# Optimization experiments

Measured on AMD Instinct MI355X. Metric: run time of the kernel, lower is better.

Reference implementation:

```python
import jax, jax.numpy as jnp
import numpy as np

N = 100000
E = 1600000
IN_C, HID_C, OUT_C = 64, 64, 40

def setup_inputs() -> dict:
    key = jax.random.key(0)
    ks = jax.random.split(key, 12)
    x = jax.random.normal(ks[0], (N, IN_C), dtype=jnp.float32)
    edge_index = jax.random.randint(ks[1], (2, E), 0, N, dtype=jnp.int32)
    def glorot(k, fan_in, fan_out):
        lim = float(np.sqrt(6.0 / (fan_in + fan_out)))
        return jax.random.uniform(k, (fan_in, fan_out), jnp.float32, -lim, lim)
    return {
        "x": x,
        "edge_index": edge_index,
        "W0_0": glorot(ks[2], IN_C, HID_C), "W1_0": glorot(ks[3], IN_C, HID_C), "b_0": jnp.zeros((HID_C,), jnp.float32),
        "W0_1": glorot(ks[4], HID_C, HID_C), "W1_1": glorot(ks[5], HID_C, HID_C), "b_1": jnp.zeros((HID_C,), jnp.float32),
        "W0_2": glorot(ks[6], HID_C, OUT_C), "W1_2": glorot(ks[7], HID_C, OUT_C), "b_2": jnp.zeros((OUT_C,), jnp.float32),
    }

def _cheb_norm(edge_index, num_nodes, dtype):
    # PyG ChebConv.__norm__ with normalization=None, edge_weight=None -> ones.
    # L = D - A; lambda_max = 2 * max(L weights); scaled: 2L/lambda_max - I.
    src, dst = edge_index[0], edge_index[1]
    w = jnp.ones((edge_index.shape[1],), dtype)
    deg = jax.ops.segment_sum(w, src, num_segments=num_nodes)
    lam = 2.0 * jnp.maximum(jnp.max(deg), jnp.max(-w))
    scale = 2.0 / lam
    norm_edge = -w * scale            # off-diagonal entries
    norm_loop = deg * scale - 1.0     # diagonal entries (self-loop mask subtracts 1)
    return norm_edge, norm_loop

def _spmm(x, src, dst, norm_edge, norm_loop, num_nodes):
    # y[i] = sum_{e: src->i} norm_e * x[src_e] + norm_loop[i] * x[i]
    msg = norm_edge[:, None] * x[src]
    return jax.ops.segment_sum(msg, dst, num_segments=num_nodes) + norm_loop[:, None] * x

def reference(x, edge_index, W0_0, W1_0, b_0, W0_1, W1_1, b_1, W0_2, W1_2, b_2):
    num_nodes = x.shape[0]
    src, dst = edge_index[0], edge_index[1]
    norm_edge, norm_loop = _cheb_norm(edge_index, num_nodes, x.dtype)

    def cheb(h, W0, W1, b):
        # K=2: out = T0(L) h W0 + T1(L) h W1 + b, T0 = I, T1 = scaled L
        Tx1 = _spmm(h, src, dst, norm_edge, norm_loop, num_nodes)
        return h @ W0 + Tx1 @ W1 + b

    h = jax.nn.relu(cheb(x, W0_0, W1_0, b_0))   # dropout is identity in eval mode
    h = jax.nn.relu(cheb(h, W0_1, W1_1, b_1))
    h = cheb(h, W0_2, W1_2, b_2)
    return jax.nn.log_softmax(h, axis=-1)
```

## Files before the change

kernel.cpp:

```cpp
#include <hip/hip_runtime.h>
#include <math.h>

#define N_NODES 100000
#define N_EDGES 1600000
#define OUTC 40
#define PAIRS40 20

#define NC 32
#define CHUNK (N_EDGES / NC)

#define RANGE_H 32768
#define NR_H 4
#define NPAD_H (NR_H * RANGE_H)

#define RANGE_F 16384
#define NR_F 7

#define SCAN_BLOCK 1024
#define SCAN_NBLK ((N_NODES + SCAN_BLOCK - 1) / SCAN_BLOCK)

typedef float vf2 __attribute__((ext_vector_type(2)));
typedef __fp16 f16x2 __attribute__((ext_vector_type(2)));

__device__ inline unsigned pack_bf16x2(float lo, float hi) {
    unsigned a = __float_as_uint(lo), b = __float_as_uint(hi);
    a = (a + 0x7fffu + ((a >> 16) & 1u)) >> 16;
    b = (b + 0x7fffu + ((b >> 16) & 1u)) & 0xffff0000u;
    return a | b;
}
__device__ inline float bf_lo(unsigned u) { return __uint_as_float(u << 16); }
__device__ inline float bf_hi(unsigned u) { return __uint_as_float(u & 0xffff0000u); }

__device__ inline unsigned pk16(float a, float b) {
    f16x2 h = __builtin_amdgcn_cvt_pkrtz(a, b);
    return __builtin_bit_cast(unsigned, h);
}
__device__ inline f16x2 uph(unsigned u) { return __builtin_bit_cast(f16x2, u); }

__device__ inline float fdot2(f16x2 a, f16x2 b, float c) {
#if __has_builtin(__builtin_amdgcn_fdot2)
    return __builtin_amdgcn_fdot2(a, b, c, false);
#else
    float d;
    asm volatile("v_dot2_f32_f16 %0, %1, %2, %3" : "=v"(d) : "v"(a), "v"(b), "v"(c));
    return d;
#endif
}

__global__ __launch_bounds__(1024) void k_hist(const int* __restrict__ src,
                                               const int* __restrict__ dst,
                                               int* __restrict__ Hs,
                                               int* __restrict__ Hd) {
    __shared__ unsigned h32[RANGE_H / 2];
    int c = blockIdx.x, r = blockIdx.y;
    const int* a = blockIdx.z ? dst : src;
    int* H = blockIdx.z ? Hd : Hs;
    for (int k = threadIdx.x; k < RANGE_H / 2; k += 1024) h32[k] = 0;
    __syncthreads();
    int r0 = r * RANGE_H;
    int e0 = c * CHUNK, e1 = e0 + CHUNK;
    for (int e = e0 + threadIdx.x; e < e1; e += 1024) {
        unsigned d = (unsigned)(a[e] - r0);
        if (d < RANGE_H) atomicAdd(&h32[d >> 1], 1u << ((d & 1) * 16));
    }
    __syncthreads();
    for (int k = threadIdx.x; k < RANGE_H; k += 1024)
        H[c * NPAD_H + r0 + k] = (int)((h32[k >> 1] >> ((k & 1) * 16)) & 0xffffu);
}

__global__ __launch_bounds__(SCAN_BLOCK) void k_scan1(const int* __restrict__ Hs,
                                                      const int* __restrict__ Hd,
                                                      int* __restrict__ rowptr,
                                                      int* __restrict__ blocksum,
                                                      int* __restrict__ deg_src,
                                                      int* __restrict__ maxdeg) {
    __shared__ int buf[2][SCAN_BLOCK];
    int t = threadIdx.x;
    int i = blockIdx.x * SCAN_BLOCK + t;
    int vs = 0, vd = 0;
    if (i < N_NODES) {
        #pragma unroll
        for (int c = 0; c < NC; c++) { vs += Hs[c * NPAD_H + i]; vd += Hd[c * NPAD_H + i]; }
        deg_src[i] = vs;
    }
    int m = vs;
    for (int off = 32; off; off >>= 1) m = max(m, __shfl_down(m, off));
    if ((t & 63) == 0) atomicMax(maxdeg, m);
    int pd = (vd + 7) & ~7;
    int cur = 0;
    buf[0][t] = pd;
    __syncthreads();
    for (int off = 1; off < SCAN_BLOCK; off <<= 1) {
        int nv = buf[cur][t];
        if (t >= off) nv += buf[cur][t - off];
        buf[1 - cur][t] = nv;
        cur = 1 - cur;
        __syncthreads();
    }
    int incl = buf[cur][t];
    if (i < N_NODES) rowptr[i + 1] = incl;
    if (t == SCAN_BLOCK - 1) blocksum[blockIdx.x] = incl;
}

__global__ __launch_bounds__(SCAN_BLOCK) void k_finalize(const int* __restrict__ blocksum,
                                                         int* __restrict__ rowptr,
                                                         int* __restrict__ Hd,
                                                         int* __restrict__ csr_src) {
    __shared__ int soff;
    int t = threadIdx.x, blk = blockIdx.x;
    if (t == 0) {
        int r = 0;
        for (int j = 0; j < blk; j++) r += blocksum[j];
        soff = r;
        if (blk == 0) rowptr[0] = 0;
    }
    __syncthreads();
    int i = blk * SCAN_BLOCK + t;
    if (i >= N_NODES) return;
    int tmp[NC];
    int s = 0;
    #pragma unroll
    for (int c = 0; c < NC; c++) { tmp[c] = Hd[c * NPAD_H + i]; s += tmp[c]; }
    int rf = rowptr[i + 1] + soff;
    rowptr[i + 1] = rf;
    int pd = (s + 7) & ~7;
    int run = rf - pd;
    #pragma unroll
    for (int c = 0; c < NC; c++) { Hd[c * NPAD_H + i] = run; run += tmp[c]; }
    for (int k = run; k < rf; k++) csr_src[k] = N_NODES;
}

__global__ __launch_bounds__(1024) void k_fill2(const int* __restrict__ src,
                                                const int* __restrict__ dst,
                                                const int* __restrict__ basepos,
                                                int* __restrict__ csr_src) {
    __shared__ int pos[RANGE_F];
    int c = blockIdx.x, r = blockIdx.y;
    int r0 = r * RANGE_F;
    for (int k = threadIdx.x; k < RANGE_F; k += 1024) pos[k] = basepos[c * NPAD_H + r0 + k];
    __syncthreads();
    int e0 = c * CHUNK, e1 = e0 + CHUNK;
    for (int e = e0 + threadIdx.x; e < e1; e += 1024) {
        unsigned d = (unsigned)(dst[e] - r0);
        if (d < RANGE_F) {
            int s = src[e];
            int p = atomicAdd(&pos[d], 1);
            csr_src[p] = s;
        }
    }
}

__global__ __launch_bounds__(256, 8) void k_gemm64(const float* __restrict__ hf,
                                                   const float* __restrict__ W0,
                                                   const float* __restrict__ W1,
                                                   const float* __restrict__ b,
                                                   const int* __restrict__ deg_src,
                                                   const int* __restrict__ maxdeg,
                                                   unsigned* __restrict__ G0b,
                                                   unsigned short* __restrict__ G1f8) {
    __shared__ uint4 swu[32 * 32];
    __shared__ unsigned shu[32 * 32];
    int t = threadIdx.x;
    const float2* W02 = (const float2*)W0;
    const float2* W12 = (const float2*)W1;
    for (int cell = t; cell < 1024; cell += 256) {
        int kp = cell >> 5, c2 = cell & 31;
        float2 a  = W02[(kp * 2) * 32 + c2];
        float2 bb = W02[(kp * 2 + 1) * 32 + c2];
        float2 cc = W12[(kp * 2) * 32 + c2];
        float2 dd = W12[(kp * 2 + 1) * 32 + c2];
        swu[cell] = make_uint4(pk16(a.x, bb.x), pk16(a.y, bb.y), pk16(cc.x, dd.x), pk16(cc.y, dd.y));
    }
    int i0 = blockIdx.x * 32;
    const float4* h4 = (const float4*)(hf + (size_t)i0 * 64);
    {
        float4 f0 = h4[t * 2], f1 = h4[t * 2 + 1];
        ((uint4*)shu)[t] = make_uint4(pk16(f0.x, f0.y), pk16(f0.z, f0.w), pk16(f1.x, f1.y), pk16(f1.z, f1.w));
    }
    if (blockIdx.x == 0 && t < 16) ((unsigned*)G1f8)[N_NODES * 16 + t] = 0;
    __syncthreads();
    int c2 = t & 31, rg = t >> 5;
    float scale = 1.0f / (float)(*maxdeg);
    float2 b2 = ((const float2*)b)[c2];
    float a0x[4], a0y[4], a1x[4], a1y[4];
    #pragma unroll
    for (int p = 0; p < 4; p++) { a0x[p] = b2.x; a0y[p] = b2.y; a1x[p] = 0.f; a1y[p] = 0.f; }
    #pragma unroll 8
    for (int kp = 0; kp < 32; kp++) {
        uint4 w = swu[kp * 32 + c2];
        f16x2 w0x = uph(w.x), w0y = uph(w.y), w1x = uph(w.z), w1y = uph(w.w);
        #pragma unroll
        for (int p = 0; p < 4; p++) {
            f16x2 h2 = uph(shu[(rg + 8 * p) * 32 + kp]);
            a0x[p] = fdot2(h2, w0x, a0x[p]);
            a0y[p] = fdot2(h2, w0y, a0y[p]);
            a1x[p] = fdot2(h2, w1x, a1x[p]);
            a1y[p] = fdot2(h2, w1y, a1y[p]);
        }
    }
    #pragma unroll
    for (int p = 0; p < 4; p++) {
        int row = i0 + rg + 8 * p;
        float nl = (float)deg_src[row] * scale - 1.0f;
        G0b[row * 32 + c2] = pack_bf16x2(a0x[p] + nl * a1x[p], a0y[p] + nl * a1y[p]);
        int pk = __builtin_amdgcn_cvt_pk_fp8_f32(a1x[p], a1y[p], 0, false);
        G1f8[row * 32 + c2] = (unsigned short)(pk & 0xffff);
    }
}

__global__ __launch_bounds__(256, 8) void k_fs64_g64(const unsigned* __restrict__ G0b_in,
                                                     const unsigned char* __restrict__ g1_in,
                                                     const int* __restrict__ rowptr,
                                                     const int* __restrict__ csr_src,
                                                     const int* __restrict__ deg_src,
                                                     const int* __restrict__ maxdeg,
                                                     const float* __restrict__ W0,
                                                     const float* __restrict__ W1,
                                                     const float* __restrict__ b,
                                                     unsigned* __restrict__ G0b_out,
                                                     unsigned short* __restrict__ G1f8_out) {
    __shared__ uint4 swu[32 * 32];
    __shared__ unsigned shu[32 * 32];
    int t = threadIdx.x;
    const float2* W02 = (const float2*)W0;
    const float2* W12 = (const float2*)W1;
    for (int cell = t; cell < 1024; cell += 256) {
        int kp = cell >> 5, c2 = cell & 31;
        float2 a  = W02[(kp * 2) * 32 + c2];
        float2 bb = W02[(kp * 2 + 1) * 32 + c2];
        float2 cc = W12[(kp * 2) * 32 + c2];
        float2 dd = W12[(kp * 2 + 1) * 32 + c2];
        swu[cell] = make_uint4(pk16(a.x, bb.x), pk16(a.y, bb.y), pk16(cc.x, dd.x), pk16(cc.y, dd.y));
    }
    int waveId = t >> 6, lane = t & 63;
    int ch = lane & 7;
    int local = waveId * 8 + (lane >> 3);
    int node = blockIdx.x * 32 + local;
    float scale = 1.0f / (float)(*maxdeg);
    int e0 = rowptr[node], e1 = rowptr[node + 1];
    int octbase = lane & 56;
    vf2 acc[4];
    acc[0] = 0.f; acc[1] = 0.f; acc[2] = 0.f; acc[3] = 0.f;
    for (int e = e0; e < e1; e += 8) {
        int idx = csr_src[e + ch];
        #pragma unroll
        for (int j = 0; j < 8; j++) {
            int s = __shfl(idx, octbase | j);
            uint2 u = ((const uint2*)(g1_in + (size_t)s * 64))[ch];
            acc[0] += __builtin_amdgcn_cvt_pk_f32_fp8((int)u.x, false);
            acc[1] += __builtin_amdgcn_cvt_pk_f32_fp8((int)u.x, true);
            acc[2] += __builtin_amdgcn_cvt_pk_f32_fp8((int)u.y, false);
            acc[3] += __builtin_amdgcn_cvt_pk_f32_fp8((int)u.y, true);
        }
    }
    uint4 g = ((const uint4*)(G0b_in + (size_t)node * 32))[ch];
    float v0 = fmaxf(bf_lo(g.x) - scale * acc[0].x, 0.f);
    float v1 = fmaxf(bf_hi(g.x) - scale * acc[0].y, 0.f);
    float v2 = fmaxf(bf_lo(g.y) - scale * acc[1].x, 0.f);
    float v3 = fmaxf(bf_hi(g.y) - scale * acc[1].y, 0.f);
    float v4 = fmaxf(bf_lo(g.z) - scale * acc[2].x, 0.f);
    float v5 = fmaxf(bf_hi(g.z) - scale * acc[2].y, 0.f);
    float v6 = fmaxf(bf_lo(g.w) - scale * acc[3].x, 0.f);
    float v7 = fmaxf(bf_hi(g.w) - scale * acc[3].y, 0.f);
    ((uint4*)shu)[local * 8 + ch] = make_uint4(pk16(v0, v1), pk16(v2, v3), pk16(v4, v5), pk16(v6, v7));
    if (blockIdx.x == 0 && t < 16) ((unsigned*)G1f8_out)[N_NODES * 16 + t] = 0;
    __syncthreads();
    int c2 = t & 31, rg = t >> 5;
    int i0 = blockIdx.x * 32;
    float2 b2 = ((const float2*)b)[c2];
    float a0x[4], a0y[4], a1x[4], a1y[4];
    #pragma unroll
    for (int p = 0; p < 4; p++) { a0x[p] = b2.x; a0y[p] = b2.y; a1x[p] = 0.f; a1y[p] = 0.f; }
    #pragma unroll 8
    for (int kp = 0; kp < 32; kp++) {
        uint4 w = swu[kp * 32 + c2];
        f16x2 w0x = uph(w.x), w0y = uph(w.y), w1x = uph(w.z), w1y = uph(w.w);
        #pragma unroll
        for (int p = 0; p < 4; p++) {
            f16x2 h2 = uph(shu[(rg + 8 * p) * 32 + kp]);
            a0x[p] = fdot2(h2, w0x, a0x[p]);
            a0y[p] = fdot2(h2, w0y, a0y[p]);
            a1x[p] = fdot2(h2, w1x, a1x[p]);
            a1y[p] = fdot2(h2, w1y, a1y[p]);
        }
    }
    #pragma unroll
    for (int p = 0; p < 4; p++) {
        int row = i0 + rg + 8 * p;
        float nl = (float)deg_src[row] * scale - 1.0f;
        G0b_out[row * 32 + c2] = pack_bf16x2(a0x[p] + nl * a1x[p], a0y[p] + nl * a1y[p]);
        int pk = __builtin_amdgcn_cvt_pk_fp8_f32(a1x[p], a1y[p], 0, false);
        G1f8_out[row * 32 + c2] = (unsigned short)(pk & 0xffff);
    }
}

__global__ __launch_bounds__(256, 8) void k_fs64_g40(const unsigned* __restrict__ G0b_in,
                                                     const unsigned char* __restrict__ g1_in,
                                                     const int* __restrict__ rowptr,
                                                     const int* __restrict__ csr_src,
                                                     const int* __restrict__ deg_src,
                                                     const int* __restrict__ maxdeg,
                                                     const float* __restrict__ W0,
                                                     const float* __restrict__ W1,
                                                     const float* __restrict__ b,
                                                     unsigned* __restrict__ G0b_out,
                                                     unsigned short* __restrict__ G1f8_out) {
    __shared__ uint4 swu[32 * PAIRS40];
    __shared__ unsigned shu[32 * 32];
    int t = threadIdx.x;
    const float2* W02 = (const float2*)W0;
    const float2* W12 = (const float2*)W1;
    for (int cell = t; cell < 32 * PAIRS40; cell += 256) {
        int kp = cell / PAIRS40, c2 = cell % PAIRS40;
        float2 a  = W02[(kp * 2) * PAIRS40 + c2];
        float2 bb = W02[(kp * 2 + 1) * PAIRS40 + c2];
        float2 cc = W12[(kp * 2) * PAIRS40 + c2];
        float2 dd = W12[(kp * 2 + 1) * PAIRS40 + c2];
        swu[cell] = make_uint4(pk16(a.x, bb.x), pk16(a.y, bb.y), pk16(cc.x, dd.x), pk16(cc.y, dd.y));
    }
    int waveId = t >> 6, lane = t & 63;
    int ch = lane & 7;
    int local = waveId * 8 + (lane >> 3);
    int node = blockIdx.x * 32 + local;
    float scale = 1.0f / (float)(*maxdeg);
    int e0 = rowptr[node], e1 = rowptr[node + 1];
    int octbase = lane & 56;
    vf2 acc[4];
    acc[0] = 0.f; acc[1] = 0.f; acc[2] = 0.f; acc[3] = 0.f;
    for (int e = e0; e < e1; e += 8) {
        int idx = csr_src[e + ch];
        #pragma unroll
        for (int j = 0; j < 8; j++) {
            int s = __shfl(idx, octbase | j);
            uint2 u = ((const uint2*)(g1_in + (size_t)s * 64))[ch];
            acc[0] += __builtin_amdgcn_cvt_pk_f32_fp8((int)u.x, false);
            acc[1] += __builtin_amdgcn_cvt_pk_f32_fp8((int)u.x, true);
            acc[2] += __builtin_amdgcn_cvt_pk_f32_fp8((int)u.y, false);
            acc[3] += __builtin_amdgcn_cvt_pk_f32_fp8((int)u.y, true);
        }
    }
    uint4 g = ((const uint4*)(G0b_in + (size_t)node * 32))[ch];
    float v0 = fmaxf(bf_lo(g.x) - scale * acc[0].x, 0.f);
    float v1 = fmaxf(bf_hi(g.x) - scale * acc[0].y, 0.f);
    float v2 = fmaxf(bf_lo(g.y) - scale * acc[1].x, 0.f);
    float v3 = fmaxf(bf_hi(g.y) - scale * acc[1].y, 0.f);
    float v4 = fmaxf(bf_lo(g.z) - scale * acc[2].x, 0.f);
    float v5 = fmaxf(bf_hi(g.z) - scale * acc[2].y, 0.f);
    float v6 = fmaxf(bf_lo(g.w) - scale * acc[3].x, 0.f);
    float v7 = fmaxf(bf_hi(g.w) - scale * acc[3].y, 0.f);
    ((uint4*)shu)[local * 8 + ch] = make_uint4(pk16(v0, v1), pk16(v2, v3), pk16(v4, v5), pk16(v6, v7));
    if (blockIdx.x == 0 && t < 10) ((unsigned*)G1f8_out)[N_NODES * 10 + t] = 0;
    __syncthreads();
    int c2 = t & 31, rg = t >> 5;
    if (c2 >= PAIRS40) return;
    int i0 = blockIdx.x * 32;
    float2 b2 = ((const float2*)b)[c2];
    float a0x[4], a0y[4], a1x[4], a1y[4];
    #pragma unroll
    for (int p = 0; p < 4; p++) { a0x[p] = b2.x; a0y[p] = b2.y; a1x[p] = 0.f; a1y[p] = 0.f; }
    #pragma unroll 8
    for (int kp = 0; kp < 32; kp++) {
        uint4 w = swu[kp * PAIRS40 + c2];
        f16x2 w0x = uph(w.x), w0y = uph(w.y), w1x = uph(w.z), w1y = uph(w.w);
        #pragma unroll
        for (int p = 0; p < 4; p++) {
            f16x2 h2 = uph(shu[(rg + 8 * p) * 32 + kp]);
            a0x[p] = fdot2(h2, w0x, a0x[p]);
            a0y[p] = fdot2(h2, w0y, a0y[p]);
            a1x[p] = fdot2(h2, w1x, a1x[p]);
            a1y[p] = fdot2(h2, w1y, a1y[p]);
        }
    }
    #pragma unroll
    for (int p = 0; p < 4; p++) {
        int row = i0 + rg + 8 * p;
        float nl = (float)deg_src[row] * scale - 1.0f;
        G0b_out[row * PAIRS40 + c2] = pack_bf16x2(a0x[p] + nl * a1x[p], a0y[p] + nl * a1y[p]);
        int pk = __builtin_amdgcn_cvt_pk_fp8_f32(a1x[p], a1y[p], 0, false);
        G1f8_out[row * PAIRS40 + c2] = (unsigned short)(pk & 0xffff);
    }
}

__global__ __launch_bounds__(256) void k_spmm40(const unsigned* __restrict__ G0b,
                                               const unsigned char* __restrict__ g1,
                                               const int* __restrict__ rowptr,
                                               const int* __restrict__ csr_src,
                                               const int* __restrict__ maxdeg,
                                               float* __restrict__ out) {
    int t = threadIdx.x;
    int waveId = t >> 6, lane = t & 63;
    int ch = lane & 7;
    bool act = ch < 5;
    int node = blockIdx.x * 32 + waveId * 8 + (lane >> 3);
    float scale = 1.0f / (float)(*maxdeg);
    int e0 = rowptr[node], e1 = rowptr[node + 1];
    int octbase = lane & 56;
    vf2 acc[4];
    acc[0] = 0.f; acc[1] = 0.f; acc[2] = 0.f; acc[3] = 0.f;
    for (int e = e0; e < e1; e += 8) {
        int idx = csr_src[e + ch];
        #pragma unroll
        for (int j = 0; j < 8; j++) {
            int s = __shfl(idx, octbase | j);
            if (act) {
                uint2 u = ((const uint2*)(g1 + (size_t)s * 40))[ch];
                acc[0] += __builtin_amdgcn_cvt_pk_f32_fp8((int)u.x, false);
                acc[1] += __builtin_amdgcn_cvt_pk_f32_fp8((int)u.x, true);
                acc[2] += __builtin_amdgcn_cvt_pk_f32_fp8((int)u.y, false);
                acc[3] += __builtin_amdgcn_cvt_pk_f32_fp8((int)u.y, true);
            }
        }
    }
    float v[8];
    float m = -INFINITY;
    if (act) {
        uint4 g = ((const uint4*)(G0b + (size_t)node * PAIRS40))[ch];
        v[0] = bf_lo(g.x) - scale * acc[0].x;
        v[1] = bf_hi(g.x) - scale * acc[0].y;
        v[2] = bf_lo(g.y) - scale * acc[1].x;
        v[3] = bf_hi(g.y) - scale * acc[1].y;
        v[4] = bf_lo(g.z) - scale * acc[2].x;
        v[5] = bf_hi(g.z) - scale * acc[2].y;
        v[6] = bf_lo(g.w) - scale * acc[3].x;
        v[7] = bf_hi(g.w) - scale * acc[3].y;
        #pragma unroll
        for (int q = 0; q < 8; q++) m = fmaxf(m, v[q]);
    }
    m = fmaxf(m, __shfl_xor(m, 1));
    m = fmaxf(m, __shfl_xor(m, 2));
    m = fmaxf(m, __shfl_xor(m, 4));
    float s = 0.f;
    if (act) {
        #pragma unroll
        for (int q = 0; q < 8; q++) s += __expf(v[q] - m);
    }
    s += __shfl_xor(s, 1);
    s += __shfl_xor(s, 2);
    s += __shfl_xor(s, 4);
    float ls = __logf(s);
    if (act) {
        float4 oA, oB;
        oA.x = v[0] - m - ls; oA.y = v[1] - m - ls; oA.z = v[2] - m - ls; oA.w = v[3] - m - ls;
        oB.x = v[4] - m - ls; oB.y = v[5] - m - ls; oB.z = v[6] - m - ls; oB.w = v[7] - m - ls;
        float4* o4 = (float4*)(out + (size_t)node * 40);
        o4[ch * 2] = oA;
        o4[ch * 2 + 1] = oB;
    }
}


extern "C" void kernel_launch(void* const* d_in, const int* in_sizes, int n_in,
                              void* d_out, int out_size, void* d_ws, size_t ws_size,
                              hipStream_t stream) {
    const float* x   = (const float*)d_in[0];
    const int* ei    = (const int*)d_in[1];
    const int* src   = ei;
    const int* dst   = ei + N_EDGES;
    const float* W0_0 = (const float*)d_in[2];
    const float* W1_0 = (const float*)d_in[3];
    const float* b_0  = (const float*)d_in[4];
    const float* W0_1 = (const float*)d_in[5];
    const float* W1_1 = (const float*)d_in[6];
    const float* b_1  = (const float*)d_in[7];
    const float* W0_2 = (const float*)d_in[8];
    const float* W1_2 = (const float*)d_in[9];
    const float* b_2  = (const float*)d_in[10];
    float* outp = (float*)d_out;

    int* ip = (int*)d_ws;
    int* deg_src  = ip;
    int* rowptr   = ip + 100000;
    int* blocksum = ip + 200064;
    int* maxdeg   = ip + 200192;
    int* csr_src  = ip + 200256;
    int* Hs       = ip + 2700256;
    int* Hd       = ip + 6894560;
    unsigned* GA0 = (unsigned*)(ip + 11088864);
    unsigned short* GA1 = (unsigned short*)(ip + 14288864);
    unsigned* GB0 = (unsigned*)(ip + 15888928);
    unsigned short* GB1 = (unsigned short*)(ip + 19088928);

    (void)hipMemsetAsync(maxdeg, 0, sizeof(int), stream);

    k_hist<<<dim3(NC, NR_H, 2), 1024, 0, stream>>>(src, dst, Hs, Hd);
    k_scan1<<<SCAN_NBLK, SCAN_BLOCK, 0, stream>>>(Hs, Hd, rowptr, blocksum, deg_src, maxdeg);
    k_finalize<<<SCAN_NBLK, SCAN_BLOCK, 0, stream>>>(blocksum, rowptr, Hd, csr_src);
    k_fill2<<<dim3(NC, NR_F), 1024, 0, stream>>>(src, dst, Hd, csr_src);

    const int GS = N_NODES / 32;

    k_gemm64<<<GS, 256, 0, stream>>>(x, W0_0, W1_0, b_0, deg_src, maxdeg, GA0, GA1);
    k_fs64_g64<<<GS, 256, 0, stream>>>(GA0, (const unsigned char*)GA1, rowptr, csr_src,
                                       deg_src, maxdeg, W0_1, W1_1, b_1, GB0, GB1);
    k_fs64_g40<<<GS, 256, 0, stream>>>(GB0, (const unsigned char*)GB1, rowptr, csr_src,
                                       deg_src, maxdeg, W0_2, W1_2, b_2, GA0, GA1);
    k_spmm40<<<GS, 256, 0, stream>>>(GA0, (const unsigned char*)GA1, rowptr, csr_src, maxdeg, outp);
}
```

Measured before the change: 323.7 us.

## Bucket nodes by padded degree so each wave gathers similar-length rows

Adds a degree-bucket count in the scan kernel, a tiny prefix kernel, and a permutation written in finalize that orders nodes by padded in-degree. The three gather/SPMM kernels then process nodes through this permutation, so the eight nodes sharing a wave have similar loop trip counts and divergence is reduced. It also prefetches the next csr index chunk in the edge loop and unrolls the fp16 dot-product GEMM by two k-steps with paired LDS loads. The cost is an extra launch, shared atomics, and scattered (non-contiguous) row reads and writes, which reduce locality.

```diff
diff --git a/kernel.cpp b/kernel.cpp
--- a/kernel.cpp
+++ b/kernel.cpp
@@ -18,6 +18,8 @@
 
 #define SCAN_BLOCK 1024
 #define SCAN_NBLK ((N_NODES + SCAN_BLOCK - 1) / SCAN_BLOCK)
+
+#define NBUCKET 16
 
 typedef float vf2 __attribute__((ext_vector_type(2)));
 typedef __fp16 f16x2 __attribute__((ext_vector_type(2)));
@@ -73,9 +75,12 @@
                                                       int* __restrict__ rowptr,
                                                       int* __restrict__ blocksum,
                                                       int* __restrict__ deg_src,
-                                                      int* __restrict__ maxdeg) {
+                                                      int* __restrict__ maxdeg,
+                                                      int* __restrict__ gcnt) {
     __shared__ int buf[2][SCAN_BLOCK];
+    __shared__ int bcnt[NBUCKET];
     int t = threadIdx.x;
+    if (t < NBUCKET) bcnt[t] = 0;
     int i = blockIdx.x * SCAN_BLOCK + t;
     int vs = 0, vd = 0;
     if (i < N_NODES) {
@@ -87,6 +92,11 @@
     for (int off = 32; off; off >>= 1) m = max(m, __shfl_down(m, off));
     if ((t & 63) == 0) atomicMax(maxdeg, m);
     int pd = (vd + 7) & ~7;
+    __syncthreads();
+    if (i < N_NODES) {
+        int k = pd >> 3; if (k > NBUCKET - 1) k = NBUCKET - 1;
+        atomicAdd(&bcnt[k], 1);
+    }
     int cur = 0;
     buf[0][t] = pd;
     __syncthreads();
@@ -100,13 +110,24 @@
     int incl = buf[cur][t];
     if (i < N_NODES) rowptr[i + 1] = incl;
     if (t == SCAN_BLOCK - 1) blocksum[blockIdx.x] = incl;
+    if (t < NBUCKET && bcnt[t]) atomicAdd(&gcnt[t], bcnt[t]);
+}
+
+__global__ void k_binit(const int* __restrict__ gcnt, int* __restrict__ gpos) {
+    if (threadIdx.x == 0) {
+        int r = 0;
+        for (int k = 0; k < NBUCKET; k++) { gpos[k] = r; r += gcnt[k]; }
+    }
 }
 
 __global__ __launch_bounds__(SCAN_BLOCK) void k_finalize(const int* __restrict__ blocksum,
                                                          int* __restrict__ rowptr,
                                                          int* __restrict__ Hd,
-                                                         int* __restrict__ csr_src) {
+                                                         int* __restrict__ csr_src,
+                                                         int* __restrict__ gpos,
+                                                         int* __restrict__ perm) {
     __shared__ int soff;
+    __shared__ int cnt[NBUCKET], base[NBUCKET];
     int t = threadIdx.x, blk = blockIdx.x;
     if (t == 0) {
         int r = 0;
@@ -114,20 +135,32 @@
         soff = r;
         if (blk == 0) rowptr[0] = 0;
     }
+    if (t < NBUCKET) cnt[t] = 0;
     __syncthreads();
     int i = blk * SCAN_BLOCK + t;
-    if (i >= N_NODES) return;
+    bool valid = i < N_NODES;
     int tmp[NC];
     int s = 0;
-    #pragma unroll
-    for (int c = 0; c < NC; c++) { tmp[c] = Hd[c * NPAD_H + i]; s += tmp[c]; }
-    int rf = rowptr[i + 1] + soff;
-    rowptr[i + 1] = rf;
+    if (valid) {
+        #pragma unroll
+        for (int c = 0; c < NC; c++) { tmp[c] = Hd[c * NPAD_H + i]; s += tmp[c]; }
+    }
     int pd = (s + 7) & ~7;
-    int run = rf - pd;
-    #pragma unroll
-    for (int c = 0; c < NC; c++) { Hd[c * NPAD_H + i] = run; run += tmp[c]; }
-    for (int k = run; k < rf; k++) csr_src[k] = N_NODES;
+    int k = pd >> 3; if (k > NBUCKET - 1) k = NBUCKET - 1;
+    int lrank = 0;
+    if (valid) lrank = atomicAdd(&cnt[k], 1);
+    __syncthreads();
+    if (t < NBUCKET && cnt[t]) base[t] = atomicAdd(&gpos[t], cnt[t]);
+    __syncthreads();
+    if (valid) {
+        perm[base[k] + lrank] = i;
+        int rf = rowptr[i + 1] + soff;
+        rowptr[i + 1] = rf;
+        int run = rf - pd;
+        #pragma unroll
+        for (int c = 0; c < NC; c++) { Hd[c * NPAD_H + i] = run; run += tmp[c]; }
+        for (int kk = run; kk < rf; kk++) csr_src[kk] = N_NODES;
+    }
 }
 
 __global__ __launch_bounds__(1024) void k_fill2(const int* __restrict__ src,
@@ -185,17 +218,22 @@
     float a0x[4], a0y[4], a1x[4], a1y[4];
     #pragma unroll
     for (int p = 0; p < 4; p++) { a0x[p] = b2.x; a0y[p] = b2.y; a1x[p] = 0.f; a1y[p] = 0.f; }
-    #pragma unroll 8
-    for (int kp = 0; kp < 32; kp++) {
-        uint4 w = swu[kp * 32 + c2];
-        f16x2 w0x = uph(w.x), w0y = uph(w.y), w1x = uph(w.z), w1y = uph(w.w);
+    #pragma unroll 4
+    for (int kp = 0; kp < 32; kp += 2) {
+        uint4 wa = swu[kp * 32 + c2];
+        uint4 wb = swu[(kp + 1) * 32 + c2];
         #pragma unroll
         for (int p = 0; p < 4; p++) {
-            f16x2 h2 = uph(shu[(rg + 8 * p) * 32 + kp]);
-            a0x[p] = fdot2(h2, w0x, a0x[p]);
-            a0y[p] = fdot2(h2, w0y, a0y[p]);
-            a1x[p] = fdot2(h2, w1x, a1x[p]);
-            a1y[p] = fdot2(h2, w1y, a1y[p]);
+            uint2 hp = ((const uint2*)(shu + (rg + 8 * p) * 32))[kp >> 1];
+            f16x2 ha = uph(hp.x), hb = uph(hp.y);
+            a0x[p] = fdot2(ha, uph(wa.x), a0x[p]);
+            a0y[p] = fdot2(ha, uph(wa.y), a0y[p]);
+            a1x[p] = fdot2(ha, uph(wa.z), a1x[p]);
+            a1y[p] = fdot2(ha, uph(wa.w), a1y[p]);
+            a0x[p] = fdot2(hb, uph(wb.x), a0x[p]);
+            a0y[p] = fdot2(hb, uph(wb.y), a0y[p]);
+            a1x[p] = fdot2(hb, uph(wb.z), a1x[p]);
+            a1y[p] = fdot2(hb, uph(wb.w), a1y[p]);
         }
     }
     #pragma unroll
@@ -214,6 +252,7 @@
                                                      const int* __restrict__ csr_src,
                                                      const int* __restrict__ deg_src,
                                                      const int* __restrict__ maxdeg,
+                                                     const int* __restrict__ perm,
                                                      const float* __restrict__ W0,
                                                      const float* __restrict__ W1,
                                                      const float* __restrict__ b,
@@ -235,14 +274,20 @@
     int waveId = t >> 6, lane = t & 63;
     int ch = lane & 7;
     int local = waveId * 8 + (lane >> 3);
-    int node = blockIdx.x * 32 + local;
+    int i0 = blockIdx.x * 32;
+    int node = perm[i0 + local];
     float scale = 1.0f / (float)(*maxdeg);
     int e0 = rowptr[node], e1 = rowptr[node + 1];
     int octbase = lane & 56;
     vf2 acc[4];
     acc[0] = 0.f; acc[1] = 0.f; acc[2] = 0.f; acc[3] = 0.f;
-    for (int e = e0; e < e1; e += 8) {
-        int idx = csr_src[e + ch];
+    int e = e0;
+    int idx = 0;
+    if (e < e1) idx = csr_src[e + ch];
+    while (e < e1) {
+        int en = e + 8;
+        int idxn = 0;
+        if (en < e1) idxn = csr_src[en + ch];
         #pragma unroll
         for (int j = 0; j < 8; j++) {
             int s = __shfl(idx, octbase | j);
@@ -252,6 +297,8 @@
             acc[2] += __builtin_amdgcn_cvt_pk_f32_fp8((int)u.y, false);
             acc[3] += __builtin_amdgcn_cvt_pk_f32_fp8((int)u.y, true);
         }
+        idx = idxn;
+        e = en;
     }
     uint4 g = ((const uint4*)(G0b_in + (size_t)node * 32))[ch];
     float v0 = fmaxf(bf_lo(g.x) - scale * acc[0].x, 0.f);
@@ -266,27 +313,31 @@
     if (blockIdx.x == 0 && t < 16) ((unsigned*)G1f8_out)[N_NODES * 16 + t] = 0;
     __syncthreads();
     int c2 = t & 31, rg = t >> 5;
-    int i0 = blockIdx.x * 32;
     float2 b2 = ((const float2*)b)[c2];
     float a0x[4], a0y[4], a1x[4], a1y[4];
     #pragma unroll
     for (int p = 0; p < 4; p++) { a0x[p] = b2.x; a0y[p] = b2.y; a1x[p] = 0.f; a1y[p] = 0.f; }
-    #pragma unroll 8
-    for (int kp = 0; kp < 32; kp++) {
-        uint4 w = swu[kp * 32 + c2];
-        f16x2 w0x = uph(w.x), w0y = uph(w.y), w1x = uph(w.z), w1y = uph(w.w);
+    #pragma unroll 4
+    for (int kp = 0; kp < 32; kp += 2) {
+        uint4 wa = swu[kp * 32 + c2];
+        uint4 wb = swu[(kp + 1) * 32 + c2];
         #pragma unroll
         for (int p = 0; p < 4; p++) {
-            f16x2 h2 = uph(shu[(rg + 8 * p) * 32 + kp]);
-            a0x[p] = fdot2(h2, w0x, a0x[p]);
-            a0y[p] = fdot2(h2, w0y, a0y[p]);
-            a1x[p] = fdot2(h2, w1x, a1x[p]);
-            a1y[p] = fdot2(h2, w1y, a1y[p]);
+            uint2 hp = ((const uint2*)(shu + (rg + 8 * p) * 32))[kp >> 1];
+            f16x2 ha = uph(hp.x), hb = uph(hp.y);
+            a0x[p] = fdot2(ha, uph(wa.x), a0x[p]);
+            a0y[p] = fdot2(ha, uph(wa.y), a0y[p]);
+            a1x[p] = fdot2(ha, uph(wa.z), a1x[p]);
+            a1y[p] = fdot2(ha, uph(wa.w), a1y[p]);
+            a0x[p] = fdot2(hb, uph(wb.x), a0x[p]);
+            a0y[p] = fdot2(hb, uph(wb.y), a0y[p]);
+            a1x[p] = fdot2(hb, uph(wb.z), a1x[p]);
+            a1y[p] = fdot2(hb, uph(wb.w), a1y[p]);
         }
     }
     #pragma unroll
     for (int p = 0; p < 4; p++) {
-        int row = i0 + rg + 8 * p;
+        int row = perm[i0 + rg + 8 * p];
         float nl = (float)deg_src[row] * scale - 1.0f;
         G0b_out[row * 32 + c2] = pack_bf16x2(a0x[p] + nl * a1x[p], a0y[p] + nl * a1y[p]);
         int pk = __builtin_amdgcn_cvt_pk_fp8_f32(a1x[p], a1y[p], 0, false);
@@ -300,6 +351,7 @@
                                                      const int* __restrict__ csr_src,
                                                      const int* __restrict__ deg_src,
                                                      const int* __restrict__ maxdeg,
+                                                     const int* __restrict__ perm,
                                                      const float* __restrict__ W0,
                                                      const float* __restrict__ W1,
                                                      const float* __restrict__ b,
@@ -321,14 +373,20 @@
     int waveId = t >> 6, lane = t & 63;
     int ch = lane & 7;
     int local = waveId * 8 + (lane >> 3);
-    int node = blockIdx.x * 32 + local;
+    int i0 = blockIdx.x * 32;
+    int node = perm[i0 + local];
     float scale = 1.0f / (float)(*maxdeg);
     int e0 = rowptr[node], e1 = rowptr[node + 1];
     int octbase = lane & 56;
     vf2 acc[4];
     acc[0] = 0.f; acc[1] = 0.f; acc[2] = 0.f; acc[3] = 0.f;
-    for (int e = e0; e < e1; e += 8) {
-        int idx = csr_src[e + ch];
+    int e = e0;
+    int idx = 0;
+    if (e < e1) idx = csr_src[e + ch];
+    while (e < e1) {
+        int en = e + 8;
+        int idxn = 0;
+        if (en < e1) idxn = csr_src[en + ch];
         #pragma unroll
         for (int j = 0; j < 8; j++) {
             int s = __shfl(idx, octbase | j);
@@ -338,6 +396,8 @@
             acc[2] += __builtin_amdgcn_cvt_pk_f32_fp8((int)u.y, false);
             acc[3] += __builtin_amdgcn_cvt_pk_f32_fp8((int)u.y, true);
         }
+        idx = idxn;
+        e = en;
     }
     uint4 g = ((const uint4*)(G0b_in + (size_t)node * 32))[ch];
     float v0 = fmaxf(bf_lo(g.x) - scale * acc[0].x, 0.f);
@@ -353,27 +413,31 @@
     __syncthreads();
     int c2 = t & 31, rg = t >> 5;
     if (c2 >= PAIRS40) return;
-    int i0 = blockIdx.x * 32;
     float2 b2 = ((const float2*)b)[c2];
     float a0x[4], a0y[4], a1x[4], a1y[4];
     #pragma unroll
     for (int p = 0; p < 4; p++) { a0x[p] = b2.x; a0y[p] = b2.y; a1x[p] = 0.f; a1y[p] = 0.f; }
-    #pragma unroll 8
-    for (int kp = 0; kp < 32; kp++) {
-        uint4 w = swu[kp * PAIRS40 + c2];
-        f16x2 w0x = uph(w.x), w0y = uph(w.y), w1x = uph(w.z), w1y = uph(w.w);
+    #pragma unroll 4
+    for (int kp = 0; kp < 32; kp += 2) {
+        uint4 wa = swu[kp * PAIRS40 + c2];
+        uint4 wb = swu[(kp + 1) * PAIRS40 + c2];
         #pragma unroll
         for (int p = 0; p < 4; p++) {
-            f16x2 h2 = uph(shu[(rg + 8 * p) * 32 + kp]);
-            a0x[p] = fdot2(h2, w0x, a0x[p]);
-            a0y[p] = fdot2(h2, w0y, a0y[p]);
-            a1x[p] = fdot2(h2, w1x, a1x[p]);
-            a1y[p] = fdot2(h2, w1y, a1y[p]);
+            uint2 hp = ((const uint2*)(shu + (rg + 8 * p) * 32))[kp >> 1];
+            f16x2 ha = uph(hp.x), hb = uph(hp.y);
+            a0x[p] = fdot2(ha, uph(wa.x), a0x[p]);
+            a0y[p] = fdot2(ha, uph(wa.y), a0y[p]);
+            a1x[p] = fdot2(ha, uph(wa.z), a1x[p]);
+            a1y[p] = fdot2(ha, uph(wa.w), a1y[p]);
+            a0x[p] = fdot2(hb, uph(wb.x), a0x[p]);
+            a0y[p] = fdot2(hb, uph(wb.y), a0y[p]);
+            a1x[p] = fdot2(hb, uph(wb.z), a1x[p]);
+            a1y[p] = fdot2(hb, uph(wb.w), a1y[p]);
         }
     }
     #pragma unroll
     for (int p = 0; p < 4; p++) {
-        int row = i0 + rg + 8 * p;
+        int row = perm[i0 + rg + 8 * p];
         float nl = (float)deg_src[row] * scale - 1.0f;
         G0b_out[row * PAIRS40 + c2] = pack_bf16x2(a0x[p] + nl * a1x[p], a0y[p] + nl * a1y[p]);
         int pk = __builtin_amdgcn_cvt_pk_fp8_f32(a1x[p], a1y[p], 0, false);
@@ -386,19 +450,25 @@
                                                const int* __restrict__ rowptr,
                                                const int* __restrict__ csr_src,
                                                const int* __restrict__ maxdeg,
+                                               const int* __restrict__ perm,
                                                float* __restrict__ out) {
     int t = threadIdx.x;
     int waveId = t >> 6, lane = t & 63;
     int ch = lane & 7;
     bool act = ch < 5;
-    int node = blockIdx.x * 32 + waveId * 8 + (lane >> 3);
+    int node = perm[blockIdx.x * 32 + waveId * 8 + (lane >> 3)];
     float scale = 1.0f / (float)(*maxdeg);
     int e0 = rowptr[node], e1 = rowptr[node + 1];
     int octbase = lane & 56;
     vf2 acc[4];
     acc[0] = 0.f; acc[1] = 0.f; acc[2] = 0.f; acc[3] = 0.f;
-    for (int e = e0; e < e1; e += 8) {
-        int idx = csr_src[e + ch];
+    int e = e0;
+    int idx = 0;
+    if (e < e1) idx = csr_src[e + ch];
+    while (e < e1) {
+        int en = e + 8;
+        int idxn = 0;
+        if (en < e1) idxn = csr_src[en + ch];
         #pragma unroll
         for (int j = 0; j < 8; j++) {
             int s = __shfl(idx, octbase | j);
@@ -410,6 +480,8 @@
                 acc[3] += __builtin_amdgcn_cvt_pk_f32_fp8((int)u.y, true);
             }
         }
+        idx = idxn;
+        e = en;
     }
     float v[8];
     float m = -INFINITY;
@@ -472,6 +544,8 @@
     int* rowptr   = ip + 100000;
     int* blocksum = ip + 200064;
     int* maxdeg   = ip + 200192;
+    int* gcnt     = ip + 200193;
+    int* gpos     = ip + 200224;
     int* csr_src  = ip + 200256;
     int* Hs       = ip + 2700256;
     int* Hd       = ip + 6894560;
@@ -479,20 +553,22 @@
     unsigned short* GA1 = (unsigned short*)(ip + 14288864);
     unsigned* GB0 = (unsigned*)(ip + 15888928);
     unsigned short* GB1 = (unsigned short*)(ip + 19088928);
-
-    (void)hipMemsetAsync(maxdeg, 0, sizeof(int), stream);
+    int* perm     = Hs;
+
+    (void)hipMemsetAsync(maxdeg, 0, 17 * sizeof(int), stream);
 
     k_hist<<<dim3(NC, NR_H, 2), 1024, 0, stream>>>(src, dst, Hs, Hd);
-    k_scan1<<<SCAN_NBLK, SCAN_BLOCK, 0, stream>>>(Hs, Hd, rowptr, blocksum, deg_src, maxdeg);
-    k_finalize<<<SCAN_NBLK, SCAN_BLOCK, 0, stream>>>(blocksum, rowptr, Hd, csr_src);
+    k_scan1<<<SCAN_NBLK, SCAN_BLOCK, 0, stream>>>(Hs, Hd, rowptr, blocksum, deg_src, maxdeg, gcnt);
+    k_binit<<<1, 64, 0, stream>>>(gcnt, gpos);
+    k_finalize<<<SCAN_NBLK, SCAN_BLOCK, 0, stream>>>(blocksum, rowptr, Hd, csr_src, gpos, perm);
     k_fill2<<<dim3(NC, NR_F), 1024, 0, stream>>>(src, dst, Hd, csr_src);
 
     const int GS = N_NODES / 32;
 
     k_gemm64<<<GS, 256, 0, stream>>>(x, W0_0, W1_0, b_0, deg_src, maxdeg, GA0, GA1);
     k_fs64_g64<<<GS, 256, 0, stream>>>(GA0, (const unsigned char*)GA1, rowptr, csr_src,
-                                       deg_src, maxdeg, W0_1, W1_1, b_1, GB0, GB1);
+                                       deg_src, maxdeg, perm, W0_1, W1_1, b_1, GB0, GB1);
     k_fs64_g40<<<GS, 256, 0, stream>>>(GB0, (const unsigned char*)GB1, rowptr, csr_src,
-                                       deg_src, maxdeg, W0_2, W1_2, b_2, GA0, GA1);
-    k_spmm40<<<GS, 256, 0, stream>>>(GA0, (const unsigned char*)GA1, rowptr, csr_src, maxdeg, outp);
-}
+                                       deg_src, maxdeg, perm, W0_2, W1_2, b_2, GA0, GA1);
+    k_spmm40<<<GS, 256, 0, stream>>>(GA0, (const unsigned char*)GA1, rowptr, csr_src, maxdeg, perm, outp);
+}
```

New measurement: 333.5 us. 3.0% more time.
